# Kernel tuning notes

Measured on AMD Instinct MI355X. Metric: run time of the kernel, lower is better.

## Reference

```python
import jax, jax.numpy as jnp
import numpy as np

B = 16
H = W = 56
C = 384
WS = 7            # window size
SS = 3            # shift size
NH = 12           # num heads
HD = C // NH      # head dim
N = WS * WS       # tokens per window (49)
NW = (H // WS) * (W // WS)  # windows per image (64)
HID = 4 * C       # MLP hidden
SCALE = HD ** -0.5
EPS = 1e-5


def _rel_pos_index():
    coords = np.stack(np.meshgrid(np.arange(WS), np.arange(WS), indexing='ij')).reshape(2, -1)
    rel = (coords[:, :, None] - coords[:, None, :]).transpose(1, 2, 0)  # [N,N,2]
    rel[:, :, 0] += WS - 1
    rel[:, :, 1] += WS - 1
    rel[:, :, 0] *= 2 * WS - 1
    return rel.sum(-1).astype(np.int32)  # [N,N] in [0, (2WS-1)^2)


def _attn_mask():
    img = np.zeros((H, W))
    cnt = 0
    for hs in (slice(0, -WS), slice(-WS, -SS), slice(-SS, None)):
        for ws in (slice(0, -WS), slice(-WS, -SS), slice(-SS, None)):
            img[hs, ws] = cnt
            cnt += 1
    mw = img.reshape(H // WS, WS, W // WS, WS).transpose(0, 2, 1, 3).reshape(-1, N)  # [NW,N]
    d = mw[:, None, :] - mw[:, :, None]  # [NW,N,N]
    return np.where(d != 0, -100.0, 0.0).astype(np.float32)


def setup_inputs() -> dict:
    key = jax.random.key(0)
    ks = jax.random.split(key, 8)
    std = 0.02
    return {
        'x': jax.random.normal(ks[0], (B, H * W, C), jnp.float32),
        'g1': jnp.ones((C,), jnp.float32),
        'b1': jnp.zeros((C,), jnp.float32),
        'qkv_w': jax.random.normal(ks[1], (C, 3 * C), jnp.float32) * std,
        'qkv_b': jnp.zeros((3 * C,), jnp.float32),
        'rpb_table': jax.random.normal(ks[2], ((2 * WS - 1) ** 2, NH), jnp.float32) * std,
        'proj_w': jax.random.normal(ks[3], (C, C), jnp.float32) * std,
        'proj_b': jnp.zeros((C,), jnp.float32),
        'g2': jnp.ones((C,), jnp.float32),
        'b2': jnp.zeros((C,), jnp.float32),
        'fc1_w': jax.random.normal(ks[4], (C, HID), jnp.float32) * std,
        'fc1_b': jnp.zeros((HID,), jnp.float32),
        'fc2_w': jax.random.normal(ks[5], (HID, C), jnp.float32) * std,
        'fc2_b': jnp.zeros((C,), jnp.float32),
        'rel_idx': jnp.asarray(_rel_pos_index()),
        'attn_mask': jnp.asarray(_attn_mask()),
    }


def _ln(x, g, b):
    m = x.mean(-1, keepdims=True)
    v = ((x - m) ** 2).mean(-1, keepdims=True)
    return (x - m) / jnp.sqrt(v + EPS) * g + b


def reference(x, g1, b1, qkv_w, qkv_b, rpb_table, proj_w, proj_b,
              g2, b2, fc1_w, fc1_b, fc2_w, fc2_b, rel_idx, attn_mask):
    shortcut = x
    h = _ln(x, g1, b1).reshape(B, H, W, C)
    # cyclic shift
    h = jnp.roll(h, (-SS, -SS), axis=(1, 2))
    # window partition -> [B*NW, N, C]
    win = h.reshape(B, H // WS, WS, W // WS, WS, C).transpose(0, 1, 3, 2, 4, 5).reshape(-1, N, C)
    # qkv
    qkv = (win @ qkv_w + qkv_b).reshape(-1, N, 3, NH, HD).transpose(2, 0, 3, 1, 4)
    q, k, v = qkv[0] * SCALE, qkv[1], qkv[2]  # [B*NW, NH, N, HD]
    attn = jnp.einsum('bhnd,bhmd->bhnm', q, k)  # [B*NW, NH, N, N]
    # relative position bias
    rpb = rpb_table[rel_idx.reshape(-1)].reshape(N, N, NH).transpose(2, 0, 1)  # [NH,N,N]
    attn = attn + rpb[None]
    # shifted-window attention mask
    attn = attn.reshape(B, NW, NH, N, N) + attn_mask[None, :, None]
    attn = jax.nn.softmax(attn.reshape(-1, NH, N, N), axis=-1)
    out = jnp.einsum('bhnm,bhmd->bhnd', attn, v).transpose(0, 2, 1, 3).reshape(-1, N, C)
    out = out @ proj_w + proj_b
    # window reverse + reverse shift
    out = out.reshape(B, H // WS, W // WS, WS, WS, C).transpose(0, 1, 3, 2, 4, 5).reshape(B, H, W, C)
    out = jnp.roll(out, (SS, SS), axis=(1, 2)).reshape(B, H * W, C)
    x = shortcut + out
    # MLP (exact GELU, as nn.GELU default)
    h2 = _ln(x, g2, b2)
    h2 = jax.nn.gelu(h2 @ fc1_w + fc1_b, approximate=False) @ fc2_w + fc2_b
    return x + h2
```

## Files before the change

### kernel.cpp

```cpp
#include <hip/hip_runtime.h>
#include <hip/hip_bf16.h>
#include <math.h>

typedef __hip_bfloat16 bf16;
typedef __attribute__((ext_vector_type(8))) short short8;
typedef __attribute__((ext_vector_type(4))) float f32x4;

#define C_DIM 384
#define SS 3
#define SCALE_ATTN 0.17677669529663687f
#define LN_EPS 1e-5f

typedef const __attribute__((address_space(1))) void g_cvoid;
typedef __attribute__((address_space(3))) void l_void;
__device__ __forceinline__ void gl_lds16(const void* g, void* l) {
    __builtin_amdgcn_global_load_lds((g_cvoid*)g, (l_void*)l, 16, 0, 0);
}

__global__ void transpose_cast_kernel(const float* __restrict__ in, bf16* __restrict__ out,
                                      int R, int Cc) {
    int idx = blockIdx.x * 256 + threadIdx.x;
    if (idx < R * Cc) {
        int r = idx / Cc, c = idx - r * Cc;
        out[(size_t)c * R + r] = __float2bfloat16(in[idx]);
    }
}

__global__ void build_bm_kernel(const float* __restrict__ rpb, const int* __restrict__ rel_idx,
                                const float* __restrict__ mask, float* __restrict__ BM) {
    int idx = blockIdx.x * 256 + threadIdx.x;
    int col = idx & 63, row = (idx >> 6) & 63;
    int h = (idx >> 12) % 12, wi = idx / (12 * 4096);
    float v = -1e30f;
    if (row < 49 && col < 49)
        v = rpb[rel_idx[row * 49 + col] * 12 + h] + mask[(size_t)wi * 2401 + row * 49 + col];
    BM[idx] = v;
}

__global__ __launch_bounds__(256)
void ln1_shift_window(const float* __restrict__ x, const float* __restrict__ g,
                      const float* __restrict__ bta, bf16* __restrict__ win) {
    int wave = threadIdx.x >> 6, lane = threadIdx.x & 63;
    int token = blockIdx.x * 4 + wave;
    int bw = token / 49, ntk = token - bw * 49;
    int bb = bw >> 6, wi = bw & 63;
    int wh = wi >> 3, wwi = wi & 7;
    int rr = ntk / 7, cc = ntk - rr * 7;
    int hs = wh * 7 + rr + SS; if (hs >= 56) hs -= 56;
    int ws = wwi * 7 + cc + SS; if (ws >= 56) ws -= 56;
    const float* src = x + ((size_t)(bb * 3136 + hs * 56 + ws)) * C_DIM;

    float v[6]; float s = 0.f, sq = 0.f;
    #pragma unroll
    for (int j = 0; j < 6; j++) {
        v[j] = src[lane + j * 64];
        s += v[j]; sq += v[j] * v[j];
    }
    #pragma unroll
    for (int o = 32; o > 0; o >>= 1) { s += __shfl_xor(s, o, 64); sq += __shfl_xor(sq, o, 64); }
    float mean = s * (1.0f / 384.0f);
    float var  = sq * (1.0f / 384.0f) - mean * mean;
    float rstd = rsqrtf(var + LN_EPS);

    bf16* dst = win + (size_t)token * C_DIM;
    #pragma unroll
    for (int j = 0; j < 6; j++) {
        int c = lane + j * 64;
        dst[c] = __float2bfloat16((v[j] - mean) * rstd * g[c] + bta[c]);
    }
}

__global__ __launch_bounds__(256)
void ln2_kernel(const float* __restrict__ xmid, const float* __restrict__ g,
                const float* __restrict__ bta, bf16* __restrict__ out) {
    int wave = threadIdx.x >> 6, lane = threadIdx.x & 63;
    int token = blockIdx.x * 4 + wave;
    const float* src = xmid + (size_t)token * C_DIM;
    float v[6]; float s = 0.f, sq = 0.f;
    #pragma unroll
    for (int j = 0; j < 6; j++) {
        v[j] = src[lane + j * 64];
        s += v[j]; sq += v[j] * v[j];
    }
    #pragma unroll
    for (int o = 32; o > 0; o >>= 1) { s += __shfl_xor(s, o, 64); sq += __shfl_xor(sq, o, 64); }
    float mean = s * (1.0f / 384.0f);
    float var  = sq * (1.0f / 384.0f) - mean * mean;
    float rstd = rsqrtf(var + LN_EPS);
    bf16* dst = out + (size_t)token * C_DIM;
    #pragma unroll
    for (int j = 0; j < 6; j++) {
        int c = lane + j * 64;
        dst[c] = __float2bfloat16((v[j] - mean) * rstd * g[c] + bta[c]);
    }
}

template <int MODE>
__global__ __launch_bounds__(512)
void gemm_kernel(const bf16* __restrict__ A, const bf16* __restrict__ BT,
                 const float* __restrict__ bias, void* __restrict__ out,
                 const float* __restrict__ resid, int M, int N, int K) {
    __shared__ bf16 As[3][8192];
    __shared__ bf16 Bs[3][4096];

    int tid = threadIdx.x;
    int wave = tid >> 6, lane = tid & 63, quad = lane >> 4, r = lane & 15;
    int wave_m = wave >> 1, wave_n = wave & 1;

    int nN = N >> 7;
    int nwg = gridDim.x;
    int bid = blockIdx.x;
    int q8 = nwg >> 3, r8 = nwg & 7;
    int xcd = bid & 7, loc = bid >> 3;
    int swz = (xcd < r8 ? xcd * (q8 + 1) : r8 * (q8 + 1) + (xcd - r8) * q8) + loc;
    int mtile = swz / nN;
    int ntile = swz - mtile * nN;
    int m0 = mtile << 8, n0 = ntile << 7;

    f32x4 acc[4][4] = {};

    auto stage = [&](int buf, int k0) {
        #pragma unroll
        for (int c = 0; c < 2; c++) {
            int ai = wave * 2 + c;
            int slot = ai * 64 + lane;
            int panel = slot >> 8, row = slot & 255;
            gl_lds16(A + (size_t)(m0 + row) * K + k0 + panel * 8,
                     &As[buf][(ai * 64) * 8]);
        }
        {
            int slot = wave * 64 + lane;
            int panel = slot >> 7, row = slot & 127;
            gl_lds16(BT + (size_t)(n0 + row) * K + k0 + panel * 8,
                     &Bs[buf][(wave * 64) * 8]);
        }
    };

    auto compute = [&](int buf) {
        short8 a[4], b[4];
        #pragma unroll
        for (int mt = 0; mt < 4; mt++)
            a[mt] = *(const short8*)&As[buf][(quad * 256 + wave_m * 64 + mt * 16 + r) * 8];
        #pragma unroll
        for (int nt = 0; nt < 4; nt++)
            b[nt] = *(const short8*)&Bs[buf][(quad * 128 + wave_n * 64 + nt * 16 + r) * 8];
        __builtin_amdgcn_s_setprio(1);
        #pragma unroll
        for (int mt = 0; mt < 4; mt++)
            #pragma unroll
            for (int nt = 0; nt < 4; nt++)
                acc[mt][nt] = __builtin_amdgcn_mfma_f32_16x16x32_bf16(
                    a[mt], b[nt], acc[mt][nt], 0, 0, 0);
        __builtin_amdgcn_s_setprio(0);
    };

    int nk = K >> 5;

    stage(0, 0);
    stage(1, 32);
    asm volatile("s_waitcnt vmcnt(3)" ::: "memory");
    __builtin_amdgcn_s_barrier();
    __builtin_amdgcn_sched_barrier(0);

    int buf = 0;
    for (int kt = 0; kt < nk; kt++) {
        int pf = kt + 2;
        int pbuf = buf + 2; if (pbuf >= 3) pbuf -= 3;
        if (pf < nk) stage(pbuf, pf << 5);
        compute(buf);
        if (kt + 1 < nk) {
            __builtin_amdgcn_sched_barrier(0);
            if (pf < nk) asm volatile("s_waitcnt vmcnt(3)" ::: "memory");
            else         asm volatile("s_waitcnt vmcnt(0)" ::: "memory");
            __builtin_amdgcn_s_barrier();
            __builtin_amdgcn_sched_barrier(0);
        }
        buf++; if (buf == 3) buf = 0;
    }

    #pragma unroll
    for (int mt = 0; mt < 4; mt++) {
        #pragma unroll
        for (int nt = 0; nt < 4; nt++) {
            int n = n0 + wave_n * 64 + nt * 16 + r;
            float bv = bias[n];
            #pragma unroll
            for (int reg = 0; reg < 4; reg++) {
                int m = m0 + wave_m * 64 + mt * 16 + quad * 4 + reg;
                float v = acc[mt][nt][reg] + bv;
                if (MODE == 0) {
                    ((bf16*)out)[(size_t)m * N + n] = __float2bfloat16(v);
                } else if (MODE == 1) {
                    float gl = 0.5f * v * (1.0f + erff(v * 0.70710678118654752f));
                    ((bf16*)out)[(size_t)m * N + n] = __float2bfloat16(gl);
                } else if (MODE == 2) {
                    int bw = m / 49, ntk = m - bw * 49;
                    int bb = bw >> 6, wi = bw & 63;
                    int wh = wi >> 3, wwi = wi & 7;
                    int rr = ntk / 7, cc = ntk - rr * 7;
                    int ho = wh * 7 + rr + SS; if (ho >= 56) ho -= 56;
                    int wo = wwi * 7 + cc + SS; if (wo >= 56) wo -= 56;
                    size_t dst = ((size_t)(bb * 3136 + ho * 56 + wo)) * C_DIM + n;
                    ((float*)out)[dst] = v + resid[dst];
                } else {
                    size_t idx = (size_t)m * N + n;
                    ((float*)out)[idx] = v + resid[idx];
                }
            }
        }
    }
}

__global__ __launch_bounds__(256)
void attn_mfma_kernel(const bf16* __restrict__ qkv, const float* __restrict__ BM,
                      bf16* __restrict__ out) {
    __shared__ bf16 P_lds[4][4096];
    __shared__ bf16 V_lds[4][2048];
    int wave = threadIdx.x >> 6, lane = threadIdx.x & 63;
    int quad = lane >> 4, m16 = lane & 15;
    int bw = blockIdx.x;
    int h = blockIdx.y * 4 + wave;
    int wi = bw & 63;

    const bf16* base = qkv + (size_t)bw * 49 * 1152 + h * 32;

    bf16* Vt = V_lds[wave];
    #pragma unroll
    for (int it = 0; it < 16; it++) {
        int idx = it * 64 + lane;
        int n = idx >> 4, dp = idx & 15;
        int d0 = dp * 2;
        unsigned val = 0;
        if (n < 49)
            val = *(const unsigned*)(base + (size_t)n * 1152 + 768 + d0);
        bf16 v0 = ((const bf16*)&val)[0], v1 = ((const bf16*)&val)[1];
        int cb = (n & 56);
        Vt[d0 * 64 + ((cb ^ ((d0 & 7) << 3)) | (n & 7))] = v0;
        int d1 = d0 + 1;
        Vt[d1 * 64 + ((cb ^ ((d1 & 7) << 3)) | (n & 7))] = v1;
    }

    short8 qf[4], kf[4];
    #pragma unroll
    for (int t = 0; t < 4; t++) {
        int row = t * 16 + m16;
        int rc = (row < 49) ? row : 0;
        qf[t] = *(const short8*)(base + (size_t)rc * 1152 + quad * 8);
        kf[t] = *(const short8*)(base + (size_t)rc * 1152 + 384 + quad * 8);
    }
    f32x4 S[4][4] = {};
    #pragma unroll
    for (int mt = 0; mt < 4; mt++)
        #pragma unroll
        for (int nt = 0; nt < 4; nt++)
            S[mt][nt] = __builtin_amdgcn_mfma_f32_16x16x32_bf16(qf[mt], kf[nt], S[mt][nt], 0, 0, 0);

    const float* bmw = BM + (((size_t)wi * 12 + h) << 12);
    bf16* Pw = P_lds[wave];
    #pragma unroll
    for (int mt = 0; mt < 4; mt++) {
        #pragma unroll
        for (int reg = 0; reg < 4; reg++) {
            int row = mt * 16 + quad * 4 + reg;
            float p[4];
            float mx = -1e30f;
            #pragma unroll
            for (int nt = 0; nt < 4; nt++) {
                int col = nt * 16 + m16;
                float s = S[mt][nt][reg] * SCALE_ATTN + bmw[row * 64 + col];
                p[nt] = s;
                mx = fmaxf(mx, s);
            }
            #pragma unroll
            for (int o = 1; o < 16; o <<= 1) mx = fmaxf(mx, __shfl_xor(mx, o, 64));
            float sm = 0.f;
            #pragma unroll
            for (int nt = 0; nt < 4; nt++) { p[nt] = __expf(p[nt] - mx); sm += p[nt]; }
            #pragma unroll
            for (int o = 1; o < 16; o <<= 1) sm += __shfl_xor(sm, o, 64);
            float inv = 1.0f / sm;
            int r7 = (row & 7) << 3;
            #pragma unroll
            for (int nt = 0; nt < 4; nt++) {
                int col = nt * 16 + m16;
                int sw = ((col & 56) ^ r7) | (col & 7);
                Pw[row * 64 + sw] = __float2bfloat16(p[nt] * inv);
            }
        }
    }

    f32x4 O[4][2] = {};
    #pragma unroll
    for (int ks = 0; ks < 2; ks++) {
        int chunk = ks * 4 + quad;
        short8 pa[4], vb[2];
        #pragma unroll
        for (int mt = 0; mt < 4; mt++) {
            int row = mt * 16 + m16;
            pa[mt] = *(const short8*)&Pw[row * 64 + ((chunk ^ (row & 7)) << 3)];
        }
        #pragma unroll
        for (int nt = 0; nt < 2; nt++) {
            int d = nt * 16 + m16;
            vb[nt] = *(const short8*)&Vt[d * 64 + ((chunk ^ (d & 7)) << 3)];
        }
        #pragma unroll
        for (int mt = 0; mt < 4; mt++)
            #pragma unroll
            for (int nt = 0; nt < 2; nt++)
                O[mt][nt] = __builtin_amdgcn_mfma_f32_16x16x32_bf16(pa[mt], vb[nt], O[mt][nt], 0, 0, 0);
    }

    bf16* orow = out + (size_t)bw * 49 * 384 + h * 32;
    #pragma unroll
    for (int mt = 0; mt < 4; mt++) {
        #pragma unroll
        for (int reg = 0; reg < 4; reg++) {
            int row = mt * 16 + quad * 4 + reg;
            if (row < 49) {
                #pragma unroll
                for (int nt = 0; nt < 2; nt++)
                    orow[(size_t)row * 384 + nt * 16 + m16] = __float2bfloat16(O[mt][nt][reg]);
            }
        }
    }
}

extern "C" void kernel_launch(void* const* d_in, const int* in_sizes, int n_in,
                              void* d_out, int out_size, void* d_ws, size_t ws_size,
                              hipStream_t stream) {
    const float* x      = (const float*)d_in[0];
    const float* g1     = (const float*)d_in[1];
    const float* b1     = (const float*)d_in[2];
    const float* qkv_w  = (const float*)d_in[3];
    const float* qkv_b  = (const float*)d_in[4];
    const float* rpb    = (const float*)d_in[5];
    const float* proj_w = (const float*)d_in[6];
    const float* proj_b = (const float*)d_in[7];
    const float* g2     = (const float*)d_in[8];
    const float* b2     = (const float*)d_in[9];
    const float* fc1_w  = (const float*)d_in[10];
    const float* fc1_b  = (const float*)d_in[11];
    const float* fc2_w  = (const float*)d_in[12];
    const float* fc2_b  = (const float*)d_in[13];
    const int*   rel_idx   = (const int*)d_in[14];
    const float* attn_mask = (const float*)d_in[15];

    const int M = 50176;

    char* ws = (char*)d_ws;
    size_t off = 0;
    bf16* bufA   = (bf16*)(ws + off); off += (size_t)M * 384 * 2;
    bf16* bufBC  = (bf16*)(ws + off); off += (size_t)M * 1536 * 2;
    float* xmid  = (float*)(ws + off); off += (size_t)M * 384 * 4;
    bf16* qkv_wT  = (bf16*)(ws + off); off += (size_t)1152 * 384 * 2;
    bf16* proj_wT = (bf16*)(ws + off); off += (size_t)384 * 384 * 2;
    bf16* fc1_wT  = (bf16*)(ws + off); off += (size_t)1536 * 384 * 2;
    bf16* fc2_wT  = (bf16*)(ws + off); off += (size_t)384 * 1536 * 2;
    float* BM = (float*)(bufBC + (size_t)M * 1152);

    build_bm_kernel<<<64 * 12 * 4096 / 256, 256, 0, stream>>>(rpb, rel_idx, attn_mask, BM);

    transpose_cast_kernel<<<(384 * 1152 + 255) / 256, 256, 0, stream>>>(qkv_w, qkv_wT, 384, 1152);
    transpose_cast_kernel<<<(384 * 384 + 255) / 256, 256, 0, stream>>>(proj_w, proj_wT, 384, 384);
    transpose_cast_kernel<<<(384 * 1536 + 255) / 256, 256, 0, stream>>>(fc1_w, fc1_wT, 384, 1536);
    transpose_cast_kernel<<<(1536 * 384 + 255) / 256, 256, 0, stream>>>(fc2_w, fc2_wT, 1536, 384);

    ln1_shift_window<<<M / 4, 256, 0, stream>>>(x, g1, b1, bufA);

    gemm_kernel<0><<<(M / 256) * (1152 / 128), 512, 0, stream>>>(
        bufA, qkv_wT, qkv_b, bufBC, nullptr, M, 1152, 384);

    attn_mfma_kernel<<<dim3(1024, 3), 256, 0, stream>>>(bufBC, BM, bufA);

    gemm_kernel<2><<<(M / 256) * (384 / 128), 512, 0, stream>>>(
        bufA, proj_wT, proj_b, xmid, x, M, 384, 384);

    ln2_kernel<<<M / 4, 256, 0, stream>>>(xmid, g2, b2, bufA);

    gemm_kernel<1><<<(M / 256) * (1536 / 128), 512, 0, stream>>>(
        bufA, fc1_wT, fc1_b, bufBC, nullptr, M, 1536, 384);

    gemm_kernel<3><<<(M / 256) * (384 / 128), 512, 0, stream>>>(
        bufBC, fc2_wT, fc2_b, d_out, xmid, M, 384, 1536);
}
```

Measured before the change: 764.3 us.

## Fuse MLP fc1+GELU+fc2 into one kernel keeping hidden activations in LDS

Replaces the two MLP GEMM launches with a single kernel in which each 64-token block computes fc1 in 128-column chunks, applies bias and exact GELU, stages the result in LDS, and immediately accumulates it into fc2. This removes the global write and re-read of the large M×1536 hidden activation buffer. The trade-off is that B operands are loaded straight from global memory without LDS staging or pipelining, and the tile is smaller (64×384 per block, with large LDS use), so MFMA efficiency and weight reuse may be worse than in the tuned GEMM.

```diff
diff --git a/kernel.cpp b/kernel.cpp
--- a/kernel.cpp
+++ b/kernel.cpp
@@ -190,9 +190,6 @@
                 float v = acc[mt][nt][reg] + bv;
                 if (MODE == 0) {
                     ((bf16*)out)[(size_t)m * N + n] = __float2bfloat16(v);
-                } else if (MODE == 1) {
-                    float gl = 0.5f * v * (1.0f + erff(v * 0.70710678118654752f));
-                    ((bf16*)out)[(size_t)m * N + n] = __float2bfloat16(gl);
                 } else if (MODE == 2) {
                     int bw = m / 49, ntk = m - bw * 49;
                     int bb = bw >> 6, wi = bw & 63;
@@ -202,10 +199,114 @@
                     int wo = wwi * 7 + cc + SS; if (wo >= 56) wo -= 56;
                     size_t dst = ((size_t)(bb * 3136 + ho * 56 + wo)) * C_DIM + n;
                     ((float*)out)[dst] = v + resid[dst];
-                } else {
-                    size_t idx = (size_t)m * N + n;
-                    ((float*)out)[idx] = v + resid[idx];
                 }
+            }
+        }
+    }
+}
+
+__global__ __launch_bounds__(256)
+void fused_mlp_kernel(const bf16* __restrict__ A, const bf16* __restrict__ W1T,
+                      const float* __restrict__ fb1, const bf16* __restrict__ W2T,
+                      const float* __restrict__ fb2, const float* __restrict__ resid,
+                      float* __restrict__ out) {
+    __shared__ bf16 A_lds[64 * 384];
+    __shared__ bf16 H_lds[2][64 * 128];
+
+    int tid = threadIdx.x;
+    int wave = tid >> 6, lane = tid & 63, quad = lane >> 4, r = lane & 15;
+    int m0 = blockIdx.x * 64;
+
+    {
+        int token = tid >> 2, part = tid & 3;
+        const bf16* src = A + (size_t)(m0 + token) * 384 + part * 96;
+        #pragma unroll
+        for (int j = 0; j < 12; j++) {
+            short8 v = *(const short8*)(src + j * 8);
+            int col = part * 96 + j * 8;
+            *(short8*)&A_lds[token * 384 + (col ^ ((token & 7) << 3))] = v;
+        }
+    }
+    __syncthreads();
+
+    f32x4 acc[4][6] = {};
+
+    int p = 0;
+    for (int hc = 0; hc < 12; hc++) {
+        f32x4 acc2[4][2] = {};
+        #pragma unroll
+        for (int ks = 0; ks < 12; ks++) {
+            short8 a[4], b[2];
+            #pragma unroll
+            for (int mt = 0; mt < 4; mt++) {
+                int row = mt * 16 + r;
+                int col = ks * 32 + quad * 8;
+                a[mt] = *(const short8*)&A_lds[row * 384 + (col ^ ((row & 7) << 3))];
+            }
+            #pragma unroll
+            for (int nt = 0; nt < 2; nt++) {
+                int n = hc * 128 + wave * 32 + nt * 16 + r;
+                b[nt] = *(const short8*)(W1T + (size_t)n * 384 + ks * 32 + quad * 8);
+            }
+            #pragma unroll
+            for (int mt = 0; mt < 4; mt++)
+                #pragma unroll
+                for (int nt = 0; nt < 2; nt++)
+                    acc2[mt][nt] = __builtin_amdgcn_mfma_f32_16x16x32_bf16(
+                        a[mt], b[nt], acc2[mt][nt], 0, 0, 0);
+        }
+        #pragma unroll
+        for (int nt = 0; nt < 2; nt++) {
+            int col = wave * 32 + nt * 16 + r;
+            float bv = fb1[hc * 128 + col];
+            #pragma unroll
+            for (int mt = 0; mt < 4; mt++) {
+                #pragma unroll
+                for (int reg = 0; reg < 4; reg++) {
+                    int row = mt * 16 + quad * 4 + reg;
+                    float v = acc2[mt][nt][reg] + bv;
+                    float gl = 0.5f * v * (1.0f + erff(v * 0.70710678118654752f));
+                    H_lds[p][row * 128 + (col ^ ((row & 7) << 3))] = __float2bfloat16(gl);
+                }
+            }
+        }
+        __syncthreads();
+
+        #pragma unroll
+        for (int ks = 0; ks < 4; ks++) {
+            short8 a2[4], b2[6];
+            #pragma unroll
+            for (int mt = 0; mt < 4; mt++) {
+                int row = mt * 16 + r;
+                int col = ks * 32 + quad * 8;
+                a2[mt] = *(const short8*)&H_lds[p][row * 128 + (col ^ ((row & 7) << 3))];
+            }
+            #pragma unroll
+            for (int nt = 0; nt < 6; nt++) {
+                int n = wave * 96 + nt * 16 + r;
+                b2[nt] = *(const short8*)(W2T + (size_t)n * 1536 + hc * 128 + ks * 32 + quad * 8);
+            }
+            #pragma unroll
+            for (int mt = 0; mt < 4; mt++)
+                #pragma unroll
+                for (int nt = 0; nt < 6; nt++)
+                    acc[mt][nt] = __builtin_amdgcn_mfma_f32_16x16x32_bf16(
+                        a2[mt], b2[nt], acc[mt][nt], 0, 0, 0);
+        }
+        p ^= 1;
+    }
+
+    #pragma unroll
+    for (int nt = 0; nt < 6; nt++) {
+        int n = wave * 96 + nt * 16 + r;
+        float bv = fb2[n];
+        #pragma unroll
+        for (int mt = 0; mt < 4; mt++) {
+            #pragma unroll
+            for (int reg = 0; reg < 4; reg++) {
+                int m = m0 + mt * 16 + quad * 4 + reg;
+                size_t idx = (size_t)m * 384 + n;
+                out[idx] = acc[mt][nt][reg] + bv + resid[idx];
             }
         }
     }
@@ -378,9 +479,6 @@
 
     ln2_kernel<<<M / 4, 256, 0, stream>>>(xmid, g2, b2, bufA);
 
-    gemm_kernel<1><<<(M / 256) * (1536 / 128), 512, 0, stream>>>(
-        bufA, fc1_wT, fc1_b, bufBC, nullptr, M, 1536, 384);
-
-    gemm_kernel<3><<<(M / 256) * (384 / 128), 512, 0, stream>>>(
-        bufBC, fc2_wT, fc2_b, d_out, xmid, M, 384, 1536);
-}
+    fused_mlp_kernel<<<M / 64, 256, 0, stream>>>(
+        bufA, fc1_wT, fc1_b, fc2_wT, fc2_b, xmid, (float*)d_out);
+}
```

Measured after the change: 832.4 us. 8.9% more time.
